# Kernel tuning notes

Hardware: AMD Instinct MI355X
Metric: run time of the kernel (lower is better)

The kernel has to match this reference:

```python
import jax, jax.numpy as jnp
import numpy as np
from jax import lax

T = 36          # number of frames (dictionary rows)
MAXITER = 100   # fista maxIter
LAMBD0 = 0.01   # base sparsity weight (scaled by 1/L as in torch code)
TOL = 1e-4      # convergence tolerance


def build_dictionary(Drr, Dtheta, n_frames):
    # Vectorized version of the Python loop over i in range(T).
    i = jnp.arange(n_frames, dtype=Drr.dtype)                     # (T,)
    powr = Drr[None, :] ** i[:, None]                             # (T,N)  Drr^i (Drr>0)
    sign = jnp.where(i[:, None] % 2 == 0, 1.0, -1.0).astype(Drr.dtype)  # (-Drr)^i = (-1)^i Drr^i
    ang = i[:, None] * Dtheta[None, :]
    cosm, sinm = jnp.cos(ang), jnp.sin(ang)
    ones = jnp.ones((n_frames, 1), Drr.dtype)
    dic = jnp.concatenate(
        [ones, powr * cosm, sign * powr * cosm, powr * sinm, sign * powr * sinm],
        axis=1)                                                   # (T, 4N+1)
    G = jnp.linalg.norm(dic, axis=0)                              # column norms
    G = jnp.where(G == 0, jnp.sqrt(jnp.asarray(n_frames, Drr.dtype)), G)
    return dic / G


def softshrink(z, lambd):
    return jnp.sign(z) * jnp.maximum(jnp.abs(z) - lambd, 0.0)


def fista(D, Y):
    # D: (T,K), Y: (B,T,P). torch broadcasts the 2D init state; we carry full (B,K,P).
    DtD = D.T @ D                                                 # (K,K)
    L = jnp.linalg.norm(DtD)      # torch.norm(DtD, 2) = flattened 2-norm (Frobenius)
    linv = 1.0 / L
    DtY = jnp.einsum('tk,btp->bkp', D, Y) * linv                  # (B,K,P)
    K = DtD.shape[0]
    A = jnp.eye(K, dtype=D.dtype) - DtD * linv                    # (K,K)
    lambd = LAMBD0 * linv
    x0 = jnp.zeros_like(DtY)

    def cond(c):
        ii, t, x, y, Ay, done = c
        return (ii < MAXITER) & jnp.logical_not(done)

    def body(c):
        ii, t, x, y, Ay_prev, done = c
        Ay = jnp.einsum('kj,bjp->bkp', A, y)                      # (B,K,P)
        x_new = softshrink(Ay + DtY, lambd)
        t_new = (1.0 + jnp.sqrt(1.0 + 4.0 * t * t)) / 2.0
        tt = (t - 1.0) / t_new
        y_new = (1.0 + tt) * x_new - tt * x
        done = (jnp.linalg.norm((x - x_new).ravel()) / K) < TOL   # device-side convergence test
        return (ii + 1, t_new, x_new, y_new, Ay, done)

    init = (jnp.asarray(0, jnp.int32), jnp.asarray(1.0, D.dtype), x0, x0, x0,
            jnp.asarray(False))
    ii, t, x, y, Ay, done = lax.while_loop(cond, body, init)
    return x, Ay


def setup_inputs() -> dict:
    key = jax.random.key(0)
    k1, k2, k3 = jax.random.split(key, 3)
    N, B, P = 40, 4, 16384
    Drr = (0.8 + 0.2 * jax.random.uniform(k1, (N,))).astype(jnp.float32)   # pole radii near 1
    Dtheta = (np.pi * jax.random.uniform(k2, (N,))).astype(jnp.float32)    # pole angles
    x = jax.random.normal(k3, (B, T, P), dtype=jnp.float32)
    return {"x": x, "Drr": Drr, "Dtheta": Dtheta}


def reference(x, Drr, Dtheta):
    D = build_dictionary(Drr, Dtheta, T)
    sparsecode, _ = fista(D, x)
    return sparsecode
```

## Files before the change

kernel.cpp:

```cpp
#include <hip/hip_runtime.h>
#include <hip/hip_bf16.h>

typedef __attribute__((ext_vector_type(8))) short bf16x8;
typedef __attribute__((ext_vector_type(4))) float f32x4;

#define NITER 100
#define WS_SCAL  5904
#define WS_TT    6016
#define WS_AH    8192
#define WS_FLOATS (8192 + 19200 + 19200)
#define BUFB 6144

__device__ __forceinline__ unsigned short f2bf(float x) {
  unsigned u = __builtin_bit_cast(unsigned, x);
  u += 0x7fffu + ((u >> 16) & 1u);
  return (unsigned short)(u >> 16);
}
__device__ __forceinline__ float bf2f(unsigned short h) {
  unsigned u = ((unsigned)h) << 16;
  return __builtin_bit_cast(float, u);
}
__device__ __forceinline__ float ubit(unsigned u) { return __builtin_bit_cast(float, u); }
__device__ __forceinline__ unsigned cvt_pk_bf16(float a, float b) {
  unsigned r;
  asm("v_cvt_pk_bf16_f32 %0, %1, %2" : "=v"(r) : "v"(a), "v"(b));
  return r;
}

__global__ __launch_bounds__(256) void prep_kernel(const float* __restrict__ Drr,
                                                   const float* __restrict__ Dth,
                                                   float* __restrict__ ws)
{
  __shared__ float sD[36 * 164];
  __shared__ float sIG[164];
  __shared__ float sRed[256];
  const int tid = (int)threadIdx.x;

  for (int idx = tid; idx < 36 * 164; idx += 256) {
    int t = idx / 164, k = idx - t * 164;
    float v = 0.0f;
    if (k == 0) v = 1.0f;
    else if (k < 161) {
      int km = k - 1, g = km / 40, n = km - g * 40;
      float pw  = powf(Drr[n], (float)t);
      float ang = (float)t * Dth[n];
      float base = ((g & 2) == 0) ? cosf(ang) : sinf(ang);
      v = pw * base;
      if ((g & 1) && (t & 1)) v = -v;
    }
    sD[idx] = v;
  }
  __syncthreads();
  if (tid < 161) {
    float s = 0.0f;
    for (int t = 0; t < 36; ++t) { float d = sD[t * 164 + tid]; s += d * d; }
    float g = sqrtf(s);
    if (g == 0.0f) g = 6.0f;
    sIG[tid] = 1.0f / g;
  }
  __syncthreads();
  for (int idx = tid; idx < 36 * 164; idx += 256) {
    int k = idx % 164;
    if (k < 161) sD[idx] *= sIG[k];
  }
  __syncthreads();
  {
    float local = 0.0f;
    for (int idx = tid; idx < 36 * 36; idx += 256) {
      int t = idx / 36, t2 = idx - t * 36;
      float dot = 0.0f;
      for (int k = 0; k < 161; ++k) dot += sD[t * 164 + k] * sD[t2 * 164 + k];
      local += dot * dot;
    }
    sRed[tid] = local;
  }
  __syncthreads();
  for (int off = 128; off > 0; off >>= 1) {
    if (tid < off) sRed[tid] += sRed[tid + off];
    __syncthreads();
  }
  const float linv = 1.0f / sqrtf(sRed[0]);

  if (blockIdx.x == 0) {
    for (int idx = tid; idx < 36 * 164; idx += 256) ws[idx] = sD[idx];
    if (tid == 0) {
      ws[WS_SCAL] = linv;
      ws[WS_SCAL + 1] = 0.01f * linv;
      float t = 1.0f;
      for (int k = 0; k < NITER; ++k) {
        float tn = 0.5f * (1.0f + sqrtf(1.0f + 4.0f * t * t));
        float tt = (t - 1.0f) / tn;
        ws[WS_TT + 2 * k]     = tt;
        ws[WS_TT + 2 * k + 1] = 1.0f + tt;
        t = tn;
      }
    }
  }
  unsigned short* AH16 = reinterpret_cast<unsigned short*>(ws + WS_AH);
  unsigned short* AL16 = AH16 + 192 * 200;
  const int ENT = (192 * 200 + (int)gridDim.x - 1) / (int)gridDim.x;
  const int base = (int)blockIdx.x * ENT;
  for (int i = tid; i < ENT; i += 256) {
    int e = base + i;
    if (e >= 192 * 200) break;
    int r = e / 200, j = e - r * 200;
    float a = 0.0f;
    if (r < 161 && j < 161) {
      float dot = 0.0f;
      for (int t = 0; t < 36; ++t) dot += sD[t * 164 + r] * sD[t * 164 + j];
      a = ((r == j) ? 1.0f : 0.0f) - dot * linv;
    }
    unsigned short ah = f2bf(a);
    AH16[e] = ah;
    AL16[e] = f2bf(a - bf2f(ah));
  }
}

template <int USE_WS>
__global__ __launch_bounds__(768, 3) void fista_kernel(
    const float* __restrict__ X, const float* __restrict__ Drr,
    const float* __restrict__ Dth, float* __restrict__ out,
    const float* __restrict__ ws)
{
  __shared__ union {
    struct { float sD[36 * 164]; float sIG[164]; float sRed[768]; } su;
    struct { unsigned char bounce[2][BUFB]; float2 tt[128]; } lp;
  } sm;
  float* sD = sm.su.sD;

  const int tid  = (int)threadIdx.x;
  const int lane = tid & 63;
  const int wv   = tid >> 6;
  const int cl   = lane & 15;
  const int hi   = lane >> 4;

  float linv, lambd;
  if constexpr (USE_WS) {
    for (int idx = tid; idx < 36 * 164; idx += 768) sD[idx] = ws[idx];
    linv  = ws[WS_SCAL];
    lambd = ws[WS_SCAL + 1];
    __syncthreads();
  } else {
    for (int idx = tid; idx < 36 * 164; idx += 768) {
      int t = idx / 164, k = idx - t * 164;
      float v = 0.0f;
      if (k == 0) v = 1.0f;
      else if (k < 161) {
        int km = k - 1, g = km / 40, n = km - g * 40;
        float pw  = powf(Drr[n], (float)t);
        float ang = (float)t * Dth[n];
        float base = ((g & 2) == 0) ? cosf(ang) : sinf(ang);
        v = pw * base;
        if ((g & 1) && (t & 1)) v = -v;
      }
      sD[idx] = v;
    }
    __syncthreads();
    if (tid < 161) {
      float s = 0.0f;
      for (int t = 0; t < 36; ++t) { float d = sD[t * 164 + tid]; s += d * d; }
      float g = sqrtf(s);
      if (g == 0.0f) g = 6.0f;
      sm.su.sIG[tid] = 1.0f / g;
    }
    __syncthreads();
    for (int idx = tid; idx < 36 * 164; idx += 768) {
      int k = idx % 164;
      if (k < 161) sD[idx] *= sm.su.sIG[k];
    }
    __syncthreads();
    {
      float local = 0.0f;
      for (int idx = tid; idx < 36 * 36; idx += 768) {
        int t = idx / 36, t2 = idx - t * 36;
        float dot = 0.0f;
        for (int k = 0; k < 161; ++k) dot += sD[t * 164 + k] * sD[t2 * 164 + k];
        local += dot * dot;
      }
      sm.su.sRed[tid] = local;
    }
    __syncthreads();
    if (tid < 256) sm.su.sRed[tid] += sm.su.sRed[tid + 256] + sm.su.sRed[tid + 512];
    __syncthreads();
    for (int off = 128; off > 0; off >>= 1) {
      if (tid < off) sm.su.sRed[tid] += sm.su.sRed[tid + off];
      __syncthreads();
    }
    linv  = 1.0f / sqrtf(sm.su.sRed[0]);
    lambd = 0.01f * linv;
  }

  bf16x8 Ah[6], Al[6];
  if constexpr (USE_WS) {
    const unsigned short* AH16 = reinterpret_cast<const unsigned short*>(ws + WS_AH);
    const unsigned short* AL16 = AH16 + 192 * 200;
    const int r = wv * 16 + cl;
    #pragma unroll
    for (int kt = 0; kt < 6; ++kt) {
      Ah[kt] = *reinterpret_cast<const bf16x8*>(AH16 + r * 200 + kt * 32 + hi * 8);
      Al[kt] = *reinterpret_cast<const bf16x8*>(AL16 + r * 200 + kt * 32 + hi * 8);
    }
  } else {
    const int r = wv * 16 + cl;
    #pragma unroll
    for (int kt = 0; kt < 6; ++kt) {
      const int k0 = kt * 32 + hi * 8;
      float acc8[8];
      #pragma unroll
      for (int j = 0; j < 8; ++j) acc8[j] = 0.0f;
      if (r < 161) {
        for (int t = 0; t < 36; ++t) {
          float vr = sD[t * 164 + r];
          #pragma unroll
          for (int j = 0; j < 8; ++j) acc8[j] += vr * sD[t * 164 + k0 + j];
        }
      }
      bf16x8 vh, vl;
      #pragma unroll
      for (int j = 0; j < 8; ++j) {
        int k = k0 + j;
        float a = 0.0f;
        if (r < 161 && k < 161) {
          a = -acc8[j] * linv;
          if (r == k) a += 1.0f;
        }
        unsigned short h = f2bf(a);
        vh[j] = (short)h;
        vl[j] = (short)f2bf(a - bf2f(h));
      }
      Ah[kt] = vh;
      Al[kt] = vl;
    }
  }

  const int c = (int)blockIdx.x * 16 + cl;
  const int b = c >> 14;
  const int p = c & 16383;
  const float* Xc = X + (size_t)b * (36 * 16384) + p;

  f32x4 P0, P1, xe;
  #pragma unroll
  for (int q = 0; q < 4; ++q) { P0[q] = 0.0f; P1[q] = 0.0f; xe[q] = 0.0f; }

  for (int t = 0; t < 36; ++t) {
    float yv = Xc[(size_t)t * 16384];
    f32x4 df = *reinterpret_cast<const f32x4*>(sD + t * 164 + wv * 16 + hi * 4);
    #pragma unroll
    for (int q = 0; q < 4; ++q) P0[q] += df[q] * yv;
  }
  #pragma unroll
  for (int q = 0; q < 4; ++q) {
    int r = wv * 16 + hi * 4 + q;
    P0[q] = (r < 161) ? P0[q] * linv : 0.0f;
  }
  __syncthreads();

  if constexpr (USE_WS) {
    const float2* wt = reinterpret_cast<const float2*>(ws + WS_TT);
    for (int i = tid; i < NITER; i += 768) sm.lp.tt[i] = wt[i];
  } else {
    if (tid == 0) {
      float t = 1.0f;
      for (int k = 0; k < NITER; ++k) {
        float tn = 0.5f * (1.0f + sqrtf(1.0f + 4.0f * t * t));
        float tt = (t - 1.0f) / tn;
        sm.lp.tt[k] = make_float2(tt, 1.0f + tt);
        t = tn;
      }
    }
  }
  __syncthreads();

  unsigned char* colb = &sm.lp.bounce[0][0] + cl * 384;
  const unsigned swz = (unsigned)((cl & 7) << 4);
  unsigned char* rdA[6];
  #pragma unroll
  for (int kt = 0; kt < 6; ++kt)
    rdA[kt] = colb + (((unsigned)(kt * 64 + hi * 16)) ^ swz);
  unsigned char* wrA = colb + (((unsigned)(wv * 32 + hi * 8)) ^ swz);

  auto step = [&](f32x4& PC, f32x4& PN, int it, int boff) {
    float2 t2 = sm.lp.tt[it];
    const float ttp = t2.x, c1 = t2.y;
    float dq_[4];
    #pragma unroll
    for (int q = 0; q < 4; ++q) {
      float u  = c1 * PC[q] - ttp * PN[q];
      float aa = fmaxf(fabsf(u) - lambd, 0.0f);
      float xn = __builtin_copysignf(aa, u);
      dq_[q] = xn - xe[q];
    }
    unsigned w0 = cvt_pk_bf16(dq_[0], dq_[1]);
    unsigned w1 = cvt_pk_bf16(dq_[2], dq_[3]);
    xe[0] += ubit(w0 << 16);
    xe[1] += ubit(w0 & 0xffff0000u);
    xe[2] += ubit(w1 << 16);
    xe[3] += ubit(w1 & 0xffff0000u);
    *reinterpret_cast<uint2*>(wrA + boff) = make_uint2(w0, w1);
    __syncthreads();
    bf16x8 bh[6];
    #pragma unroll
    for (int kt = 0; kt < 6; ++kt)
      bh[kt] = *reinterpret_cast<const bf16x8*>(rdA[kt] + boff);
    f32x4 acc = PC;
    #pragma unroll
    for (int kt = 0; kt < 6; ++kt) {
      acc = __builtin_amdgcn_mfma_f32_16x16x32_bf16(Ah[kt], bh[kt], acc, 0, 0, 0);
      acc = __builtin_amdgcn_mfma_f32_16x16x32_bf16(Al[kt], bh[kt], acc, 0, 0, 0);
    }
    PN = acc;
  };

  #pragma unroll 1
  for (int j = 0; j < NITER / 2; ++j) {
    step(P0, P1, 2 * j, 0);
    step(P1, P0, 2 * j + 1, BUFB);
  }

  float* op = out + (size_t)b * (161 * 16384) + p;
  #pragma unroll
  for (int q = 0; q < 4; ++q) {
    int r = wv * 16 + hi * 4 + q;
    if (r < 161) op[(size_t)r * 16384] = xe[q];
  }
}

extern "C" void kernel_launch(void* const* d_in, const int* in_sizes, int n_in,
                              void* d_out, int out_size, void* d_ws, size_t ws_size,
                              hipStream_t stream) {
  const float* X   = (const float*)d_in[0];
  const float* Drr = (const float*)d_in[1];
  const float* Dth = (const float*)d_in[2];
  float* out = (float*)d_out;
  (void)in_sizes; (void)n_in; (void)out_size;

  if (ws_size >= (size_t)WS_FLOATS * sizeof(float)) {
    float* ws = (float*)d_ws;
    prep_kernel<<<dim3(64), dim3(256), 0, stream>>>(Drr, Dth, ws);
    fista_kernel<1><<<dim3(4096), dim3(768), 0, stream>>>(X, Drr, Dth, out, ws);
  } else {
    fista_kernel<0><<<dim3(4096), dim3(768), 0, stream>>>(X, Drr, Dth, out, nullptr);
  }
}
```

Measured before the change: 1.341 ms.

## Halve workgroup size, give each wave two row tiles sharing B-fragment loads

Each wave now computes two 16-row tiles of the 192x192 iteration matrix instead of one, so the workgroup shrinks from 12 to 6 waves. Each bf16 fragment read from LDS feeds four MFMAs instead of two, which halves LDS read traffic per iteration and the number of waves meeting at each barrier. The prep kernel now stores A in fp32 and every block does the hi/lo bf16 split itself. The trade-off is doubled register pressure per thread for the A fragments and accumulators, which may lower occupancy, plus a longer serial MFMA chain per wave.

```diff
diff --git a/kernel.cpp b/kernel.cpp
--- a/kernel.cpp
+++ b/kernel.cpp
@@ -7,9 +7,9 @@
 #define NITER 100
 #define WS_SCAL  5904
 #define WS_TT    6016
-#define WS_AH    8192
-#define WS_FLOATS (8192 + 19200 + 19200)
-#define BUFB 6144
+#define WS_A     8192
+#define WS_FLOATS (8192 + 192*200)
+#define BUF1 6144
 
 __device__ __forceinline__ unsigned short f2bf(float x) {
   unsigned u = __builtin_bit_cast(unsigned, x);
@@ -96,8 +96,6 @@
       }
     }
   }
-  unsigned short* AH16 = reinterpret_cast<unsigned short*>(ws + WS_AH);
-  unsigned short* AL16 = AH16 + 192 * 200;
   const int ENT = (192 * 200 + (int)gridDim.x - 1) / (int)gridDim.x;
   const int base = (int)blockIdx.x * ENT;
   for (int i = tid; i < ENT; i += 256) {
@@ -110,21 +108,19 @@
       for (int t = 0; t < 36; ++t) dot += sD[t * 164 + r] * sD[t * 164 + j];
       a = ((r == j) ? 1.0f : 0.0f) - dot * linv;
     }
-    unsigned short ah = f2bf(a);
-    AH16[e] = ah;
-    AL16[e] = f2bf(a - bf2f(ah));
+    ws[WS_A + e] = a;
   }
 }
 
 template <int USE_WS>
-__global__ __launch_bounds__(768, 3) void fista_kernel(
+__global__ __launch_bounds__(384, 3) void fista_kernel(
     const float* __restrict__ X, const float* __restrict__ Drr,
     const float* __restrict__ Dth, float* __restrict__ out,
     const float* __restrict__ ws)
 {
   __shared__ union {
-    struct { float sD[36 * 164]; float sIG[164]; float sRed[768]; } su;
-    struct { unsigned char bounce[2][BUFB]; float2 tt[128]; } lp;
+    struct { float sD[36 * 164]; float sIG[164]; float sRed[384]; } su;
+    struct { unsigned char bounce[2][BUF1]; float2 tt[112]; } lp;
   } sm;
   float* sD = sm.su.sD;
 
@@ -136,12 +132,12 @@
 
   float linv, lambd;
   if constexpr (USE_WS) {
-    for (int idx = tid; idx < 36 * 164; idx += 768) sD[idx] = ws[idx];
+    for (int idx = tid; idx < 36 * 164; idx += 384) sD[idx] = ws[idx];
     linv  = ws[WS_SCAL];
     lambd = ws[WS_SCAL + 1];
     __syncthreads();
   } else {
-    for (int idx = tid; idx < 36 * 164; idx += 768) {
+    for (int idx = tid; idx < 36 * 164; idx += 384) {
       int t = idx / 164, k = idx - t * 164;
       float v = 0.0f;
       if (k == 0) v = 1.0f;
@@ -164,14 +160,14 @@
       sm.su.sIG[tid] = 1.0f / g;
     }
     __syncthreads();
-    for (int idx = tid; idx < 36 * 164; idx += 768) {
+    for (int idx = tid; idx < 36 * 164; idx += 384) {
       int k = idx % 164;
       if (k < 161) sD[idx] *= sm.su.sIG[k];
     }
     __syncthreads();
     {
       float local = 0.0f;
-      for (int idx = tid; idx < 36 * 36; idx += 768) {
+      for (int idx = tid; idx < 36 * 36; idx += 384) {
         int t = idx / 36, t2 = idx - t * 36;
         float dot = 0.0f;
         for (int k = 0; k < 161; ++k) dot += sD[t * 164 + k] * sD[t2 * 164 + k];
@@ -180,9 +176,9 @@
       sm.su.sRed[tid] = local;
     }
     __syncthreads();
-    if (tid < 256) sm.su.sRed[tid] += sm.su.sRed[tid + 256] + sm.su.sRed[tid + 512];
-    __syncthreads();
-    for (int off = 128; off > 0; off >>= 1) {
+    if (tid < 128) sm.su.sRed[tid] += sm.su.sRed[tid + 128] + sm.su.sRed[tid + 256];
+    __syncthreads();
+    for (int off = 64; off > 0; off >>= 1) {
       if (tid < off) sm.su.sRed[tid] += sm.su.sRed[tid + off];
       __syncthreads();
     }
@@ -190,46 +186,61 @@
     lambd = 0.01f * linv;
   }
 
-  bf16x8 Ah[6], Al[6];
+  bf16x8 Ah[2][6], Al[2][6];
   if constexpr (USE_WS) {
-    const unsigned short* AH16 = reinterpret_cast<const unsigned short*>(ws + WS_AH);
-    const unsigned short* AL16 = AH16 + 192 * 200;
-    const int r = wv * 16 + cl;
-    #pragma unroll
-    for (int kt = 0; kt < 6; ++kt) {
-      Ah[kt] = *reinterpret_cast<const bf16x8*>(AH16 + r * 200 + kt * 32 + hi * 8);
-      Al[kt] = *reinterpret_cast<const bf16x8*>(AL16 + r * 200 + kt * 32 + hi * 8);
+    #pragma unroll
+    for (int tau = 0; tau < 2; ++tau) {
+      const int r = (2 * wv + tau) * 16 + cl;
+      #pragma unroll
+      for (int kt = 0; kt < 6; ++kt) {
+        const float* ap = ws + WS_A + r * 200 + kt * 32 + hi * 8;
+        f32x4 a0 = *reinterpret_cast<const f32x4*>(ap);
+        f32x4 a1 = *reinterpret_cast<const f32x4*>(ap + 4);
+        float av[8] = {a0[0], a0[1], a0[2], a0[3], a1[0], a1[1], a1[2], a1[3]};
+        bf16x8 vh, vl;
+        #pragma unroll
+        for (int j = 0; j < 8; ++j) {
+          unsigned short h = f2bf(av[j]);
+          vh[j] = (short)h;
+          vl[j] = (short)f2bf(av[j] - bf2f(h));
+        }
+        Ah[tau][kt] = vh;
+        Al[tau][kt] = vl;
+      }
     }
   } else {
-    const int r = wv * 16 + cl;
-    #pragma unroll
-    for (int kt = 0; kt < 6; ++kt) {
-      const int k0 = kt * 32 + hi * 8;
-      float acc8[8];
+    #pragma unroll
+    for (int tau = 0; tau < 2; ++tau) {
+      const int r = (2 * wv + tau) * 16 + cl;
       #pragma unroll
-      for (int j = 0; j < 8; ++j) acc8[j] = 0.0f;
-      if (r < 161) {
-        for (int t = 0; t < 36; ++t) {
-          float vr = sD[t * 164 + r];
-          #pragma unroll
-          for (int j = 0; j < 8; ++j) acc8[j] += vr * sD[t * 164 + k0 + j];
+      for (int kt = 0; kt < 6; ++kt) {
+        const int k0 = kt * 32 + hi * 8;
+        float acc8[8];
+        #pragma unroll
+        for (int j = 0; j < 8; ++j) acc8[j] = 0.0f;
+        if (r < 161) {
+          for (int t = 0; t < 36; ++t) {
+            float vr = sD[t * 164 + r];
+            #pragma unroll
+            for (int j = 0; j < 8; ++j) acc8[j] += vr * sD[t * 164 + k0 + j];
+          }
         }
-      }
-      bf16x8 vh, vl;
-      #pragma unroll
-      for (int j = 0; j < 8; ++j) {
-        int k = k0 + j;
-        float a = 0.0f;
-        if (r < 161 && k < 161) {
-          a = -acc8[j] * linv;
-          if (r == k) a += 1.0f;
+        bf16x8 vh, vl;
+        #pragma unroll
+        for (int j = 0; j < 8; ++j) {
+          int k = k0 + j;
+          float a = 0.0f;
+          if (r < 161 && k < 161) {
+            a = -acc8[j] * linv;
+            if (r == k) a += 1.0f;
+          }
+          unsigned short h = f2bf(a);
+          vh[j] = (short)h;
+          vl[j] = (short)f2bf(a - bf2f(h));
         }
-        unsigned short h = f2bf(a);
-        vh[j] = (short)h;
-        vl[j] = (short)f2bf(a - bf2f(h));
-      }
-      Ah[kt] = vh;
-      Al[kt] = vl;
+        Ah[tau][kt] = vh;
+        Al[tau][kt] = vl;
+      }
     }
   }
 
@@ -238,26 +249,33 @@
   const int p = c & 16383;
   const float* Xc = X + (size_t)b * (36 * 16384) + p;
 
-  f32x4 P0, P1, xe;
-  #pragma unroll
-  for (int q = 0; q < 4; ++q) { P0[q] = 0.0f; P1[q] = 0.0f; xe[q] = 0.0f; }
+  f32x4 P0[2], P1[2], xe[2];
+  #pragma unroll
+  for (int tau = 0; tau < 2; ++tau)
+    #pragma unroll
+    for (int q = 0; q < 4; ++q) { P0[tau][q] = 0.0f; P1[tau][q] = 0.0f; xe[tau][q] = 0.0f; }
 
   for (int t = 0; t < 36; ++t) {
     float yv = Xc[(size_t)t * 16384];
-    f32x4 df = *reinterpret_cast<const f32x4*>(sD + t * 164 + wv * 16 + hi * 4);
-    #pragma unroll
-    for (int q = 0; q < 4; ++q) P0[q] += df[q] * yv;
-  }
-  #pragma unroll
-  for (int q = 0; q < 4; ++q) {
-    int r = wv * 16 + hi * 4 + q;
-    P0[q] = (r < 161) ? P0[q] * linv : 0.0f;
-  }
+    #pragma unroll
+    for (int tau = 0; tau < 2; ++tau) {
+      f32x4 df = *reinterpret_cast<const f32x4*>(sD + t * 164 + (2 * wv + tau) * 16 + hi * 4);
+      #pragma unroll
+      for (int q = 0; q < 4; ++q) P0[tau][q] += df[q] * yv;
+    }
+  }
+  #pragma unroll
+  for (int tau = 0; tau < 2; ++tau)
+    #pragma unroll
+    for (int q = 0; q < 4; ++q) {
+      int r = (2 * wv + tau) * 16 + hi * 4 + q;
+      P0[tau][q] = (r < 161) ? P0[tau][q] * linv : 0.0f;
+    }
   __syncthreads();
 
   if constexpr (USE_WS) {
     const float2* wt = reinterpret_cast<const float2*>(ws + WS_TT);
-    for (int i = tid; i < NITER; i += 768) sm.lp.tt[i] = wt[i];
+    for (int i = tid; i < NITER; i += 384) sm.lp.tt[i] = wt[i];
   } else {
     if (tid == 0) {
       float t = 1.0f;
@@ -277,52 +295,60 @@
   #pragma unroll
   for (int kt = 0; kt < 6; ++kt)
     rdA[kt] = colb + (((unsigned)(kt * 64 + hi * 16)) ^ swz);
-  unsigned char* wrA = colb + (((unsigned)(wv * 32 + hi * 8)) ^ swz);
-
-  auto step = [&](f32x4& PC, f32x4& PN, int it, int boff) {
+  unsigned char* wrA[2];
+  #pragma unroll
+  for (int tau = 0; tau < 2; ++tau)
+    wrA[tau] = colb + (((unsigned)((2 * wv + tau) * 32 + hi * 8)) ^ swz);
+
+  auto step = [&](f32x4 (&PC)[2], f32x4 (&PN)[2], int it, int boff) {
     float2 t2 = sm.lp.tt[it];
     const float ttp = t2.x, c1 = t2.y;
-    float dq_[4];
-    #pragma unroll
-    for (int q = 0; q < 4; ++q) {
-      float u  = c1 * PC[q] - ttp * PN[q];
-      float aa = fmaxf(fabsf(u) - lambd, 0.0f);
-      float xn = __builtin_copysignf(aa, u);
-      dq_[q] = xn - xe[q];
-    }
-    unsigned w0 = cvt_pk_bf16(dq_[0], dq_[1]);
-    unsigned w1 = cvt_pk_bf16(dq_[2], dq_[3]);
-    xe[0] += ubit(w0 << 16);
-    xe[1] += ubit(w0 & 0xffff0000u);
-    xe[2] += ubit(w1 << 16);
-    xe[3] += ubit(w1 & 0xffff0000u);
-    *reinterpret_cast<uint2*>(wrA + boff) = make_uint2(w0, w1);
-    __syncthreads();
-    bf16x8 bh[6];
-    #pragma unroll
-    for (int kt = 0; kt < 6; ++kt)
-      bh[kt] = *reinterpret_cast<const bf16x8*>(rdA[kt] + boff);
-    f32x4 acc = PC;
+    #pragma unroll
+    for (int tau = 0; tau < 2; ++tau) {
+      float dq_[4];
+      #pragma unroll
+      for (int q = 0; q < 4; ++q) {
+        float u  = c1 * PC[tau][q] - ttp * PN[tau][q];
+        float aa = fmaxf(fabsf(u) - lambd, 0.0f);
+        float xn = __builtin_copysignf(aa, u);
+        dq_[q] = xn - xe[tau][q];
+      }
+      unsigned w0 = cvt_pk_bf16(dq_[0], dq_[1]);
+      unsigned w1 = cvt_pk_bf16(dq_[2], dq_[3]);
+      xe[tau][0] += ubit(w0 << 16);
+      xe[tau][1] += ubit(w0 & 0xffff0000u);
+      xe[tau][2] += ubit(w1 << 16);
+      xe[tau][3] += ubit(w1 & 0xffff0000u);
+      *reinterpret_cast<uint2*>(wrA[tau] + boff) = make_uint2(w0, w1);
+    }
+    __syncthreads();
+    f32x4 acc0 = PC[0], acc1 = PC[1];
     #pragma unroll
     for (int kt = 0; kt < 6; ++kt) {
-      acc = __builtin_amdgcn_mfma_f32_16x16x32_bf16(Ah[kt], bh[kt], acc, 0, 0, 0);
-      acc = __builtin_amdgcn_mfma_f32_16x16x32_bf16(Al[kt], bh[kt], acc, 0, 0, 0);
-    }
-    PN = acc;
+      bf16x8 bh = *reinterpret_cast<const bf16x8*>(rdA[kt] + boff);
+      acc0 = __builtin_amdgcn_mfma_f32_16x16x32_bf16(Ah[0][kt], bh, acc0, 0, 0, 0);
+      acc0 = __builtin_amdgcn_mfma_f32_16x16x32_bf16(Al[0][kt], bh, acc0, 0, 0, 0);
+      acc1 = __builtin_amdgcn_mfma_f32_16x16x32_bf16(Ah[1][kt], bh, acc1, 0, 0, 0);
+      acc1 = __builtin_amdgcn_mfma_f32_16x16x32_bf16(Al[1][kt], bh, acc1, 0, 0, 0);
+    }
+    PN[0] = acc0;
+    PN[1] = acc1;
   };
 
   #pragma unroll 1
   for (int j = 0; j < NITER / 2; ++j) {
     step(P0, P1, 2 * j, 0);
-    step(P1, P0, 2 * j + 1, BUFB);
+    step(P1, P0, 2 * j + 1, BUF1);
   }
 
   float* op = out + (size_t)b * (161 * 16384) + p;
   #pragma unroll
-  for (int q = 0; q < 4; ++q) {
-    int r = wv * 16 + hi * 4 + q;
-    if (r < 161) op[(size_t)r * 16384] = xe[q];
-  }
+  for (int tau = 0; tau < 2; ++tau)
+    #pragma unroll
+    for (int q = 0; q < 4; ++q) {
+      int r = (2 * wv + tau) * 16 + hi * 4 + q;
+      if (r < 161) op[(size_t)r * 16384] = xe[tau][q];
+    }
 }
 
 extern "C" void kernel_launch(void* const* d_in, const int* in_sizes, int n_in,
@@ -337,8 +363,8 @@
   if (ws_size >= (size_t)WS_FLOATS * sizeof(float)) {
     float* ws = (float*)d_ws;
     prep_kernel<<<dim3(64), dim3(256), 0, stream>>>(Drr, Dth, ws);
-    fista_kernel<1><<<dim3(4096), dim3(768), 0, stream>>>(X, Drr, Dth, out, ws);
+    fista_kernel<1><<<dim3(4096), dim3(384), 0, stream>>>(X, Drr, Dth, out, ws);
   } else {
-    fista_kernel<0><<<dim3(4096), dim3(768), 0, stream>>>(X, Drr, Dth, out, nullptr);
-  }
-}
+    fista_kernel<0><<<dim3(4096), dim3(384), 0, stream>>>(X, Drr, Dth, out, nullptr);
+  }
+}
```

Measured after the change: 2.215 ms. 1.65x slower.
